# Kernel optimization log

Hardware: AMD Instinct MI355X
Metric: run time of the kernel (lower is better)

The kernel has to match this reference:

```python
import jax, jax.numpy as jnp
import numpy as np

D_MODEL = 1024
NUM_HEADS = 16
SEQ = 2048
BATCH = 4
THETA = 10000.0
D_K = D_MODEL // NUM_HEADS


def setup_inputs() -> dict:
    key = jax.random.key(0)
    k1, k2, k3, k4, k5 = jax.random.split(key, 5)
    std = np.sqrt(2.0 / (D_MODEL + D_MODEL))
    x = jax.random.normal(k1, (BATCH, SEQ, D_MODEL), dtype=jnp.float32)
    wq = jax.random.normal(k2, (D_MODEL, D_MODEL), dtype=jnp.float32) * std
    wk = jax.random.normal(k3, (D_MODEL, D_MODEL), dtype=jnp.float32) * std
    wv = jax.random.normal(k4, (D_MODEL, D_MODEL), dtype=jnp.float32) * std
    wo = jax.random.normal(k5, (D_MODEL, D_MODEL), dtype=jnp.float32) * std
    token_positions = jnp.arange(SEQ, dtype=jnp.int32)
    return {"x": x, "wq": wq, "wk": wk, "wv": wv, "wo": wo,
            "token_positions": token_positions}


def _apply_rope(t, cos, sin):
    # t: (b, h, s, d_k); cos/sin: (s, d_k/2) -> broadcast over (b, h)
    pairs = t.reshape(*t.shape[:-1], D_K // 2, 2)
    x0, x1 = pairs[..., 0], pairs[..., 1]
    r0 = x0 * cos - x1 * sin
    r1 = x0 * sin + x1 * cos
    return jnp.stack((r0, r1), axis=-1).reshape(t.shape)


def reference(x, wq, wk, wv, wo, token_positions):
    b, s, d = x.shape
    h, dk = NUM_HEADS, D_K

    def split_heads(y):  # (b, s, d) -> (b, h, s, d_k)
        return y.reshape(b, s, h, dk).transpose(0, 2, 1, 3)

    q = split_heads(x @ wq.T)
    k = split_heads(x @ wk.T)
    v = split_heads(x @ wv.T)

    # RoPE tables: angles_j = theta^{-(2j)/d_k}, j = 0..d_k/2-1
    inv_freq = 1.0 / (THETA ** (jnp.arange(0, dk, 2, dtype=jnp.float32) / dk))
    ang = token_positions.astype(jnp.float32)[:, None] * inv_freq[None, :]  # (s, d_k/2)
    cos, sin = jnp.cos(ang), jnp.sin(ang)
    q = _apply_rope(q, cos, sin)
    k = _apply_rope(k, cos, sin)

    scores = jnp.einsum('bhqd,bhkd->bhqk', q, k) / jnp.sqrt(jnp.float32(dk))
    causal = jnp.tril(jnp.ones((s, s), dtype=bool))
    scores = jnp.where(causal, scores, -jnp.inf)
    attn = jax.nn.softmax(scores, axis=-1)
    out = jnp.einsum('bhqk,bhkd->bhqd', attn, v)  # (b, h, s, d_k)
    out = out.transpose(0, 2, 1, 3).reshape(b, s, d)
    return out @ wo.T
```

## Files before the change

### kernel.cpp

```cpp
#include <hip/hip_runtime.h>
#include <stdint.h>

#define B_   4
#define S_   2048
#define H_   16
#define DK_  64
#define DM_  1024
#define M_   (B_ * S_)

typedef __attribute__((ext_vector_type(4)))  float f32x4;
typedef __attribute__((ext_vector_type(16))) float f32x16;
typedef __attribute__((ext_vector_type(8)))  short s16x8;

#define SCQ 0.18033688011112042f

__device__ __forceinline__ uint16_t f2bf(float f) {
    union { float f; uint32_t u; } v; v.f = f;
    uint32_t u = v.u;
    uint32_t r = (u + 0x7FFFu + ((u >> 16) & 1u)) >> 16;
    return (uint16_t)r;
}
__device__ __forceinline__ float bf2f(uint16_t h) {
    union { uint32_t u; float f; } v; v.u = ((uint32_t)h) << 16;
    return v.f;
}
__device__ __forceinline__ uint32_t cvt_pk_bf16(float lo, float hi) {
    uint32_t r;
    asm("v_cvt_pk_bf16_f32 %0, %1, %2" : "=v"(r) : "v"(lo), "v"(hi));
    return r;
}

__device__ __forceinline__ void gload_lds16(const uint16_t* g, uint16_t* l) {
    __builtin_amdgcn_global_load_lds(
        (const __attribute__((address_space(1))) void*)g,
        (__attribute__((address_space(3))) void*)l, 16, 0, 0);
}

__global__ __launch_bounds__(256) void cvt_bf16(const float* __restrict__ in,
                                                uint16_t* __restrict__ out, int n) {
    int i = (blockIdx.x * 256 + threadIdx.x) * 4;
    if (i >= n) return;
    float4 v = *reinterpret_cast<const float4*>(in + i);
    ushort4 o;
    o.x = f2bf(v.x); o.y = f2bf(v.y); o.z = f2bf(v.z); o.w = f2bf(v.w);
    *reinterpret_cast<ushort4*>(out + i) = o;
}

__global__ __launch_bounds__(256) void cvt_w4(const float* __restrict__ w0,
                                              const float* __restrict__ w1,
                                              const float* __restrict__ w2,
                                              const float* __restrict__ w3,
                                              uint16_t* __restrict__ o0,
                                              uint16_t* __restrict__ o1,
                                              uint16_t* __restrict__ o2,
                                              uint16_t* __restrict__ o3) {
    const size_t NW = (size_t)DM_ * DM_;
    size_t i = ((size_t)blockIdx.x * 256 + threadIdx.x) * 4;
    int sel = (int)(i >> 20);
    size_t off = i & (NW - 1);
    const float* in = sel == 0 ? w0 : sel == 1 ? w1 : sel == 2 ? w2 : w3;
    uint16_t* out   = sel == 0 ? o0 : sel == 1 ? o1 : sel == 2 ? o2 : o3;
    float4 v = *reinterpret_cast<const float4*>(in + off);
    ushort4 o;
    o.x = f2bf(v.x); o.y = f2bf(v.y); o.z = f2bf(v.z); o.w = f2bf(v.w);
    *reinterpret_cast<ushort4*>(out + off) = o;
}

__global__ __launch_bounds__(256) void gemm_qkv(const uint16_t* __restrict__ xb,
                                                const uint16_t* __restrict__ wq,
                                                const uint16_t* __restrict__ wk,
                                                const uint16_t* __restrict__ wv,
                                                uint16_t* __restrict__ qout,
                                                uint16_t* __restrict__ kout,
                                                uint16_t* __restrict__ vout) {
    __shared__ uint16_t Al[2][128 * 32];
    __shared__ uint16_t Bl[2][128 * 32];
    const int K = DM_;
    const int lane = threadIdx.x & 63;
    const int w    = threadIdx.x >> 6;
    const int wr   = w >> 1, wc = w & 1;
    const int sel  = blockIdx.x >> 3;
    const int np   = blockIdx.x & 7;
    const int y    = blockIdx.y;
    const int lr   = lane & 15;
    const int lg   = lane >> 4;

    const uint16_t* Aptr; const uint16_t* Bptr;
    int m0, n0;
    if (sel == 2) { Aptr = wv; Bptr = xb; m0 = np * 128; n0 = y * 128; }
    else          { Aptr = xb; Bptr = sel ? wk : wq; m0 = y * 128; n0 = np * 128; }

    const int srow = w * 32 + (lane >> 2);
    const int scol = (((lane & 3) ^ ((lane >> 2) & 3))) * 8;
    const uint16_t* Ag = Aptr + (size_t)(m0 + srow) * K + scol;
    const uint16_t* Bg = Bptr + (size_t)(n0 + srow) * K + scol;
    const int loff = w * 32 * 32;
    const int rsw  = (lr & 3);

    f32x4 acc[4][4] = {};
#pragma unroll
    for (int i = 0; i < 2; ++i) {
        gload_lds16(Ag + (size_t)i * 16 * K, &Al[0][loff + i * 16 * 32]);
        gload_lds16(Bg + (size_t)i * 16 * K, &Bl[0][loff + i * 16 * 32]);
    }

    int cur = 0;
    for (int k0 = 0; k0 < K; k0 += 32) {
        __syncthreads();
        if (k0 + 32 < K) {
            const int nb = cur ^ 1, k2 = k0 + 32;
#pragma unroll
            for (int i = 0; i < 2; ++i) {
                gload_lds16(Ag + (size_t)i * 16 * K + k2, &Al[nb][loff + i * 16 * 32]);
                gload_lds16(Bg + (size_t)i * 16 * K + k2, &Bl[nb][loff + i * 16 * 32]);
            }
        }
        s16x8 af[4], bfr[4];
#pragma unroll
        for (int i = 0; i < 4; ++i)
            af[i] = *reinterpret_cast<const s16x8*>(
                &Al[cur][(wr * 64 + i * 16 + lr) * 32 + (lg ^ rsw) * 8]);
#pragma unroll
        for (int j = 0; j < 4; ++j)
            bfr[j] = *reinterpret_cast<const s16x8*>(
                &Bl[cur][(wc * 64 + j * 16 + lr) * 32 + (lg ^ rsw) * 8]);
#pragma unroll
        for (int i = 0; i < 4; ++i)
#pragma unroll
            for (int j = 0; j < 4; ++j)
                acc[i][j] = __builtin_amdgcn_mfma_f32_16x16x32_bf16(af[i], bfr[j],
                                                                    acc[i][j], 0, 0, 0);
        cur ^= 1;
    }

#pragma unroll
    for (int i = 0; i < 4; ++i)
#pragma unroll
        for (int j = 0; j < 4; ++j)
#pragma unroll
            for (int r = 0; r < 4; ++r) {
                int row = m0 + wr * 64 + i * 16 + lg * 4 + r;
                int col = n0 + wc * 64 + j * 16 + lr;
                float v = acc[i][j][r];
                if (sel == 2) {
                    int h = row >> 6,  dk = row & 63;
                    int b = col >> 11, s = col & (S_ - 1);
                    vout[(((size_t)(b * H_ + h)) * DK_ + dk) * S_ + s] = f2bf(v);
                } else {
                    int b = row >> 11, s = row & (S_ - 1);
                    int h = col >> 6,  dk = col & 63;
                    uint16_t bv = f2bf(sel ? v : v * SCQ);
                    (sel ? kout : qout)[(((size_t)(b * H_ + h)) * S_ + s) * DK_ + dk] = bv;
                }
            }
}

__global__ __launch_bounds__(256) void gemm_out(const uint16_t* __restrict__ A,
                                                const uint16_t* __restrict__ Bm,
                                                float* __restrict__ Cout,
                                                int M, int N, int K) {
    __shared__ uint16_t Al[2][128 * 32];
    __shared__ uint16_t Bl[2][128 * 32];
    const int lane = threadIdx.x & 63;
    const int w    = threadIdx.x >> 6;
    const int wr   = w >> 1, wc = w & 1;
    const int m0   = blockIdx.x * 128;
    const int n0   = blockIdx.y * 128;
    const int lr   = lane & 15;
    const int lg   = lane >> 4;

    const int srow = w * 32 + (lane >> 2);
    const int scol = (((lane & 3) ^ ((lane >> 2) & 3))) * 8;
    const uint16_t* Ag = A  + (size_t)(m0 + srow) * K + scol;
    const uint16_t* Bg = Bm + (size_t)(n0 + srow) * K + scol;
    const int loff = w * 32 * 32;
    const int rsw  = (lr & 3);

    f32x4 acc[4][4] = {};
#pragma unroll
    for (int i = 0; i < 2; ++i) {
        gload_lds16(Ag + (size_t)i * 16 * K, &Al[0][loff + i * 16 * 32]);
        gload_lds16(Bg + (size_t)i * 16 * K, &Bl[0][loff + i * 16 * 32]);
    }

    int cur = 0;
    for (int k0 = 0; k0 < K; k0 += 32) {
        __syncthreads();
        if (k0 + 32 < K) {
            const int nb = cur ^ 1, k2 = k0 + 32;
#pragma unroll
            for (int i = 0; i < 2; ++i) {
                gload_lds16(Ag + (size_t)i * 16 * K + k2, &Al[nb][loff + i * 16 * 32]);
                gload_lds16(Bg + (size_t)i * 16 * K + k2, &Bl[nb][loff + i * 16 * 32]);
            }
        }
        s16x8 af[4], bfr[4];
#pragma unroll
        for (int i = 0; i < 4; ++i)
            af[i] = *reinterpret_cast<const s16x8*>(
                &Al[cur][(wr * 64 + i * 16 + lr) * 32 + (lg ^ rsw) * 8]);
#pragma unroll
        for (int j = 0; j < 4; ++j)
            bfr[j] = *reinterpret_cast<const s16x8*>(
                &Bl[cur][(wc * 64 + j * 16 + lr) * 32 + (lg ^ rsw) * 8]);
#pragma unroll
        for (int i = 0; i < 4; ++i)
#pragma unroll
            for (int j = 0; j < 4; ++j)
                acc[i][j] = __builtin_amdgcn_mfma_f32_16x16x32_bf16(af[i], bfr[j],
                                                                    acc[i][j], 0, 0, 0);
        cur ^= 1;
    }

#pragma unroll
    for (int i = 0; i < 4; ++i)
#pragma unroll
        for (int j = 0; j < 4; ++j)
#pragma unroll
            for (int r = 0; r < 4; ++r) {
                int row = m0 + wr * 64 + i * 16 + lg * 4 + r;
                int col = n0 + wc * 64 + j * 16 + lr;
                Cout[(size_t)row * N + col] = acc[i][j][r];
            }
}

__global__ __launch_bounds__(256) void rope_kernel(uint16_t* __restrict__ a,
                                                   const int* __restrict__ pos,
                                                   int npairs) {
    int t = blockIdx.x * 256 + threadIdx.x;
    if (t >= npairs) return;
    int j = t & 31;
    int s = (t >> 5) & (S_ - 1);
    float p   = (float)pos[s];
    float inv = exp2f(-(float)j * (13.287712379549449f / 32.0f));
    float ang = p * inv;
    float sn, c;
    sincosf(ang, &sn, &c);
    uint32_t pr = *reinterpret_cast<uint32_t*>(a + (size_t)2 * t);
    float x0 = bf2f((uint16_t)(pr & 0xFFFF));
    float x1 = bf2f((uint16_t)(pr >> 16));
    float r0 = x0 * c - x1 * sn;
    float r1 = x0 * sn + x1 * c;
    uint32_t ot = (uint32_t)f2bf(r0) | ((uint32_t)f2bf(r1) << 16);
    *reinterpret_cast<uint32_t*>(a + (size_t)2 * t) = ot;
}

__global__ __launch_bounds__(256, 2) void flash_attn(const uint16_t* __restrict__ qg,
                                                     const uint16_t* __restrict__ kg,
                                                     const uint16_t* __restrict__ vtg,
                                                     uint16_t* __restrict__ attn) {
    __shared__ __align__(16) uint16_t Kl[2][4096];
    __shared__ __align__(16) uint16_t Vl[2][4096];
    const int lane = threadIdx.x & 63;
    const int w    = threadIdx.x >> 6;
    const int ql   = lane & 31;
    const int hi   = lane >> 5;
    const int id   = blockIdx.x;
    const int bh   = (id & 7) * 8 + ((id >> 3) & 7);
    const int s    = 15 - (id >> 6);
    const int b    = bh >> 4, hh = bh & 15;

    const uint16_t* kb_ = kg  + (size_t)bh * S_ * DK_;
    const uint16_t* vb_ = vtg + (size_t)bh * DK_ * S_;

    char* obb = (char*)&Kl[0][0] + w * 4096;
    const int swz = (ql & 7) << 4;

    const int q0 = s * 128 + w * 32;
    const int rowg  = q0 + ql;
    const int ntmax = 2 * s + 2;

    const int srow = lane >> 3;
    const int scol = ((lane & 7) ^ srow) << 3;

    const uint16_t* qp = qg + ((size_t)bh * S_ + q0 + ql) * DK_ + hi * 8;
    s16x8 qf[4];
#pragma unroll
    for (int kk = 0; kk < 4; ++kk)
        qf[kk] = *reinterpret_cast<const s16x8*>(qp + kk * 16);

    f32x16 o0 = {}, o1 = {};
    float l_l = 0.f;

#pragma unroll
    for (int i = 0; i < 2; ++i) {
        gload_lds16(kb_ + (size_t)(w * 16 + i * 8 + srow) * DK_ + scol, &Kl[0][w * 1024 + i * 512]);
        gload_lds16(vb_ + (size_t)(w * 16 + i * 8 + srow) * S_  + scol, &Vl[0][w * 1024 + i * 512]);
    }

    for (int t = 0; t < ntmax; ++t) {
        const int kt  = t * 64;
        const int cur = t & 1;
        __syncthreads();
        if (t + 1 < ntmax) {
            const int kt2 = kt + 64, nb = cur ^ 1;
#pragma unroll
            for (int i = 0; i < 2; ++i) {
                gload_lds16(kb_ + (size_t)(kt2 + w * 16 + i * 8 + srow) * DK_ + scol,
                            &Kl[nb][w * 1024 + i * 512]);
                gload_lds16(vb_ + (size_t)(w * 16 + i * 8 + srow) * S_ + kt2 + scol,
                            &Vl[nb][w * 1024 + i * 512]);
            }
        }
        if (kt > q0 + 31) continue;

        s16x8 kf[8];
#pragma unroll
        for (int kb2 = 0; kb2 < 2; ++kb2)
#pragma unroll
            for (int kk = 0; kk < 4; ++kk)
                kf[kb2 * 4 + kk] = *reinterpret_cast<const s16x8*>(
                    &Kl[cur][(kb2 * 32 + ql) * 64 + (((kk * 32 + hi * 16) ^ swz) >> 1)]);

        f32x16 sc0 = {}, sc1 = {};
        __builtin_amdgcn_s_setprio(1);
#pragma unroll
        for (int kk = 0; kk < 4; ++kk)
            sc0 = __builtin_amdgcn_mfma_f32_32x32x16_bf16(kf[kk], qf[kk], sc0, 0, 0, 0);
#pragma unroll
        for (int kk = 0; kk < 4; ++kk)
            sc1 = __builtin_amdgcn_mfma_f32_32x32x16_bf16(kf[4 + kk], qf[kk], sc1, 0, 0, 0);
        __builtin_amdgcn_s_setprio(0);

        if (kt + 63 > q0) {
            const int keybase = kt + 4 * hi;
#pragma unroll
            for (int r = 0; r < 16; ++r) {
                const int cr = (r & 3) + 8 * (r >> 2);
                if (keybase + cr > rowg)      sc0[r] = -3e38f;
                if (keybase + cr + 32 > rowg) sc1[r] = -3e38f;
            }
        }

#pragma unroll
        for (int r = 0; r < 16; ++r) {
            float p0 = exp2f(sc0[r]);
            float p1 = exp2f(sc1[r]);
            sc0[r] = p0; sc1[r] = p1;
            l_l += p0 + p1;
        }

        s16x8 pf[4];
        {
            union PW { uint32_t u[4]; s16x8 v; };
#pragma unroll
            for (int half = 0; half < 2; ++half) {
                const f32x16& e = half ? sc1 : sc0;
#pragma unroll
                for (int sl = 0; sl < 2; ++sl) {
                    const int rb = sl * 8;
                    uint32_t a0 = cvt_pk_bf16(e[rb + 0], e[rb + 1]);
                    uint32_t b0 = cvt_pk_bf16(e[rb + 4], e[rb + 5]);
                    uint32_t a1 = cvt_pk_bf16(e[rb + 2], e[rb + 3]);
                    uint32_t b1 = cvt_pk_bf16(e[rb + 6], e[rb + 7]);
                    asm("v_permlane32_swap_b32 %0, %1" : "+v"(a0), "+v"(b0));
                    asm("v_permlane32_swap_b32 %0, %1" : "+v"(a1), "+v"(b1));
                    PW pw; pw.u[0] = a0; pw.u[1] = a1; pw.u[2] = b0; pw.u[3] = b1;
                    pf[half * 2 + sl] = pw.v;
                }
            }
        }

        s16x8 vf[8];
#pragma unroll
        for (int db = 0; db < 2; ++db)
#pragma unroll
            for (int ks = 0; ks < 4; ++ks)
                vf[db * 4 + ks] = *reinterpret_cast<const s16x8*>(
                    &Vl[cur][(db * 32 + ql) * 64 + (((ks * 32 + hi * 16) ^ swz) >> 1)]);

        __builtin_amdgcn_s_setprio(1);
#pragma unroll
        for (int ks = 0; ks < 4; ++ks) {
            o0 = __builtin_amdgcn_mfma_f32_32x32x16_bf16(vf[ks],     pf[ks], o0, 0, 0, 0);
            o1 = __builtin_amdgcn_mfma_f32_32x32x16_bf16(vf[4 + ks], pf[ks], o1, 0, 0, 0);
        }
        __builtin_amdgcn_s_setprio(0);
    }

    __syncthreads();

    l_l += __shfl_xor(l_l, 32);
    float rinv = 1.0f / l_l;

#pragma unroll
    for (int db = 0; db < 2; ++db) {
        const f32x16& o = db ? o1 : o0;
#pragma unroll
        for (int rq = 0; rq < 4; ++rq) {
            uint2 val;
            val.x = cvt_pk_bf16(o[4 * rq + 0] * rinv, o[4 * rq + 1] * rinv);
            val.y = cvt_pk_bf16(o[4 * rq + 2] * rinv, o[4 * rq + 3] * rinv);
            int colb = (db * 32 + 8 * rq + 4 * hi) * 2;
            *reinterpret_cast<uint2*>(obb + ql * 128 + (colb ^ swz)) = val;
        }
    }
    uint16_t* orow = attn + ((size_t)b * S_ + q0 + ql) * DM_ + hh * 64 + hi * 32;
#pragma unroll
    for (int i = 0; i < 4; ++i) {
        int colb = hi * 64 + i * 16;
        s16x8 vrow = *reinterpret_cast<const s16x8*>(obb + ql * 128 + (colb ^ swz));
        *reinterpret_cast<s16x8*>(orow + i * 8) = vrow;
    }
}

extern "C" void kernel_launch(void* const* d_in, const int* in_sizes, int n_in,
                              void* d_out, int out_size, void* d_ws, size_t ws_size,
                              hipStream_t stream) {
    (void)in_sizes; (void)n_in; (void)out_size;
    const float* x   = (const float*)d_in[0];
    const float* wq  = (const float*)d_in[1];
    const float* wk  = (const float*)d_in[2];
    const float* wv  = (const float*)d_in[3];
    const float* wo  = (const float*)d_in[4];
    const int* tpos  = (const int*)d_in[5];
    float* out = (float*)d_out;

    const size_t NX = (size_t)M_ * DM_;
    const size_t NW = (size_t)DM_ * DM_;
    const size_t need = (NX + 4 * NW + 4 * NX) * sizeof(uint16_t);
    if (ws_size < need) return;

    uint16_t* ws  = (uint16_t*)d_ws;
    uint16_t* xb  = ws;
    uint16_t* wqb = xb + NX;
    uint16_t* wkb = wqb + NW;
    uint16_t* wvb = wkb + NW;
    uint16_t* wob = wvb + NW;
    uint16_t* qb  = wob + NW;
    uint16_t* kb  = qb + NX;
    uint16_t* vtb = kb + NX;
    uint16_t* ab  = vtb + NX;

    cvt_bf16<<<(int)(NX / 1024), 256, 0, stream>>>(x, xb, (int)NX);
    cvt_w4<<<(int)(4 * NW / 1024), 256, 0, stream>>>(wq, wk, wv, wo, wqb, wkb, wvb, wob);

    gemm_qkv<<<dim3(24, M_ / 128), 256, 0, stream>>>(xb, wqb, wkb, wvb, qb, kb, vtb);

    int npairs = 2 * B_ * H_ * S_ * (DK_ / 2);
    rope_kernel<<<npairs / 256, 256, 0, stream>>>(qb, tpos, npairs);

    flash_attn<<<dim3(1024), 256, 0, stream>>>(qb, kb, vtb, ab);

    gemm_out<<<dim3(M_ / 128, DM_ / 128), 256, 0, stream>>>(ab, wob, out, M_, DM_, DM_);
}
```

Baseline: 198.3 us.

## Merge conversion kernels, raise GEMM occupancy bounds, use fast sin/cos in RoPE

Folds the x and weight fp32-to-bf16 conversions into one launch, removing a kernel boundary. Adds a min-blocks-per-CU hint of 4 to both GEMM kernels so the compiler caps register use for higher occupancy. Replaces sincosf in the RoPE kernel with the __sinf/__cosf intrinsics. The fast intrinsics lose accuracy for large angles (positions up to 2047), and the occupancy hint may cause register spills.

```diff
diff --git a/kernel.cpp b/kernel.cpp
--- a/kernel.cpp
+++ b/kernel.cpp
@@ -36,43 +36,41 @@
         (__attribute__((address_space(3))) void*)l, 16, 0, 0);
 }
 
-__global__ __launch_bounds__(256) void cvt_bf16(const float* __restrict__ in,
-                                                uint16_t* __restrict__ out, int n) {
-    int i = (blockIdx.x * 256 + threadIdx.x) * 4;
-    if (i >= n) return;
-    float4 v = *reinterpret_cast<const float4*>(in + i);
-    ushort4 o;
-    o.x = f2bf(v.x); o.y = f2bf(v.y); o.z = f2bf(v.z); o.w = f2bf(v.w);
-    *reinterpret_cast<ushort4*>(out + i) = o;
-}
-
-__global__ __launch_bounds__(256) void cvt_w4(const float* __restrict__ w0,
-                                              const float* __restrict__ w1,
-                                              const float* __restrict__ w2,
-                                              const float* __restrict__ w3,
-                                              uint16_t* __restrict__ o0,
-                                              uint16_t* __restrict__ o1,
-                                              uint16_t* __restrict__ o2,
-                                              uint16_t* __restrict__ o3) {
+__global__ __launch_bounds__(256) void cvt_all(const float* __restrict__ x,
+                                               const float* __restrict__ w0,
+                                               const float* __restrict__ w1,
+                                               const float* __restrict__ w2,
+                                               const float* __restrict__ w3,
+                                               uint16_t* __restrict__ xo,
+                                               uint16_t* __restrict__ o0,
+                                               uint16_t* __restrict__ o1,
+                                               uint16_t* __restrict__ o2,
+                                               uint16_t* __restrict__ o3) {
+    const size_t NX = (size_t)M_ * DM_;
     const size_t NW = (size_t)DM_ * DM_;
     size_t i = ((size_t)blockIdx.x * 256 + threadIdx.x) * 4;
-    int sel = (int)(i >> 20);
-    size_t off = i & (NW - 1);
-    const float* in = sel == 0 ? w0 : sel == 1 ? w1 : sel == 2 ? w2 : w3;
-    uint16_t* out   = sel == 0 ? o0 : sel == 1 ? o1 : sel == 2 ? o2 : o3;
+    const float* in; uint16_t* out; size_t off;
+    if (i < NX) { in = x; out = xo; off = i; }
+    else {
+        size_t j = i - NX;
+        int sel = (int)(j >> 20);
+        off = j & (NW - 1);
+        in  = sel == 0 ? w0 : sel == 1 ? w1 : sel == 2 ? w2 : w3;
+        out = sel == 0 ? o0 : sel == 1 ? o1 : sel == 2 ? o2 : o3;
+    }
     float4 v = *reinterpret_cast<const float4*>(in + off);
     ushort4 o;
     o.x = f2bf(v.x); o.y = f2bf(v.y); o.z = f2bf(v.z); o.w = f2bf(v.w);
     *reinterpret_cast<ushort4*>(out + off) = o;
 }
 
-__global__ __launch_bounds__(256) void gemm_qkv(const uint16_t* __restrict__ xb,
-                                                const uint16_t* __restrict__ wq,
-                                                const uint16_t* __restrict__ wk,
-                                                const uint16_t* __restrict__ wv,
-                                                uint16_t* __restrict__ qout,
-                                                uint16_t* __restrict__ kout,
-                                                uint16_t* __restrict__ vout) {
+__global__ __launch_bounds__(256, 4) void gemm_qkv(const uint16_t* __restrict__ xb,
+                                                   const uint16_t* __restrict__ wq,
+                                                   const uint16_t* __restrict__ wk,
+                                                   const uint16_t* __restrict__ wv,
+                                                   uint16_t* __restrict__ qout,
+                                                   uint16_t* __restrict__ kout,
+                                                   uint16_t* __restrict__ vout) {
     __shared__ uint16_t Al[2][128 * 32];
     __shared__ uint16_t Bl[2][128 * 32];
     const int K = DM_;
@@ -155,10 +153,10 @@
             }
 }
 
-__global__ __launch_bounds__(256) void gemm_out(const uint16_t* __restrict__ A,
-                                                const uint16_t* __restrict__ Bm,
-                                                float* __restrict__ Cout,
-                                                int M, int N, int K) {
+__global__ __launch_bounds__(256, 4) void gemm_out(const uint16_t* __restrict__ A,
+                                                   const uint16_t* __restrict__ Bm,
+                                                   float* __restrict__ Cout,
+                                                   int M, int N, int K) {
     __shared__ uint16_t Al[2][128 * 32];
     __shared__ uint16_t Bl[2][128 * 32];
     const int lane = threadIdx.x & 63;
@@ -234,8 +232,8 @@
     float p   = (float)pos[s];
     float inv = exp2f(-(float)j * (13.287712379549449f / 32.0f));
     float ang = p * inv;
-    float sn, c;
-    sincosf(ang, &sn, &c);
+    float sn = __sinf(ang);
+    float c  = __cosf(ang);
     uint32_t pr = *reinterpret_cast<uint32_t*>(a + (size_t)2 * t);
     float x0 = bf2f((uint16_t)(pr & 0xFFFF));
     float x1 = bf2f((uint16_t)(pr >> 16));
@@ -432,8 +430,8 @@
     uint16_t* vtb = kb + NX;
     uint16_t* ab  = vtb + NX;
 
-    cvt_bf16<<<(int)(NX / 1024), 256, 0, stream>>>(x, xb, (int)NX);
-    cvt_w4<<<(int)(4 * NW / 1024), 256, 0, stream>>>(wq, wk, wv, wo, wqb, wkb, wvb, wob);
+    cvt_all<<<(int)((NX + 4 * NW) / 1024), 256, 0, stream>>>(x, wq, wk, wv, wo,
+                                                             xb, wqb, wkb, wvb, wob);
 
     gemm_qkv<<<dim3(24, M_ / 128), 256, 0, stream>>>(xb, wqb, wkb, wvb, qb, kb, vtb);
 
```

Result: faster. 193.5 us (-2.4%).
